# Optimization experiments

Measured on AMD Instinct MI355X. Metric: run time of the kernel, lower is better.

## Reference

```python
import jax, jax.numpy as jnp
import numpy as np

DELTA = 1e-3  # inverse-distance kernel smoothing from NEC paper
NUM_NEIGHBOURS = 50


def setup_inputs() -> dict:
    key = jax.random.key(0)
    k1, k2, k3 = jax.random.split(key, 3)
    B, C, D = 1024, 500000, 64
    return {
        "keys": jax.random.normal(k1, (B, D), dtype=jnp.float32),
        "table_keys": jax.random.normal(k2, (C, D), dtype=jnp.float32),
        "table_values": jax.random.normal(k3, (C,), dtype=jnp.float32),
    }


def reference(keys, table_keys, table_values):
    # Brute-force kNN search: squared L2 distances [B, C]
    d2 = (
        jnp.sum(keys * keys, axis=1, keepdims=True)
        - 2.0 * (keys @ table_keys.T)
        + jnp.sum(table_keys * table_keys, axis=1)[None, :]
    )
    _, idx = jax.lax.top_k(-d2, NUM_NEIGHBOURS)  # [B, K] smallest distances

    neighbours = table_keys[idx]  # [B, K, D] gather
    # recompute exact squared distances against gathered neighbours
    sq = jnp.sum((keys[:, None, :] - neighbours) ** 2, axis=2)  # [B, K]
    w = 1.0 / (sq + DELTA)
    w = w / jnp.sum(w, axis=1, keepdims=True)
    v = table_values[idx]  # [B, K]
    return jnp.sum(w * v, axis=1)  # [B]
```

## Files before the change

### kernel.cpp

```cpp
#include <hip/hip_runtime.h>
#include <math.h>


#define DELTA_SMOOTH 1e-3f
#define K_NEIGH 50
#define MAXCAP 8192
#define NBINS 256
#define MARGIN_T 1.5f
#define MARGIN_Q 26
#define RPB 1024
#define QTILE 512
#define SDEPTH 6
#define LW 768
#define CVL 2048
#define S_SAMP 8192
#define T_SAMP 8
#define FSAMPLE 2048
#define FTARGET 6
#define FMARGIN 0.75f
#define FQB 4

typedef __attribute__((ext_vector_type(8))) short short8;
typedef __attribute__((ext_vector_type(4))) float f32x4;
typedef __attribute__((address_space(1))) const unsigned int g_u32;
typedef __attribute__((address_space(3))) unsigned int l_u32;

__device__ __forceinline__ unsigned f2bf(float f) {
  unsigned u = __float_as_uint(f);
  return ((u + 0x7fffu + ((u >> 16) & 1u)) >> 16) & 0xffffu;
}

__global__ __launch_bounds__(512, 4) void convert_qthresh(
    const float* __restrict__ tk, uint4* __restrict__ tkbf,
    float* __restrict__ tnh2, const float* __restrict__ keys,
    unsigned short* __restrict__ dsamp, int C, int padded, int convB) {
  __shared__ __align__(16) unsigned char bstage[64 * 128];
  __shared__ float tnh_lds[64];
  int tid = threadIdx.x;

  if (blockIdx.x < (unsigned)convB) {
    int t = blockIdx.x * 512 + tid;
    int r = t >> 3;
    if (r >= padded) return;
    int c = t & 7;
    int rs = r < C ? r : C - 1;
    const float4* src = (const float4*)(tk + (size_t)rs * 64 + c * 8);
    float4 a = src[0], b = src[1];
    float sq = a.x * a.x + a.y * a.y + a.z * a.z + a.w * a.w
             + b.x * b.x + b.y * b.y + b.z * b.z + b.w * b.w;
    sq += __shfl_xor(sq, 1); sq += __shfl_xor(sq, 2); sq += __shfl_xor(sq, 4);
    if (c == 0) tnh2[r] = (r < C) ? sq * 0.5f : 3e38f;
    uint4 u;
    u.x = f2bf(a.x) | (f2bf(a.y) << 16);
    u.y = f2bf(a.z) | (f2bf(a.w) << 16);
    u.z = f2bf(b.x) | (f2bf(b.y) << 16);
    u.w = f2bf(b.z) | (f2bf(b.w) << 16);
    tkbf[(size_t)(r >> 6) * 512 + (r & 63) * 8 + (c ^ (r & 7))] = u;
    return;
  }

  int bid = blockIdx.x - convB;
  int qt = bid & 1;
  int chunk = bid >> 1;
  int qbase = qt * 512;
  int rstart = chunk * 64;
  int lane = tid & 63, wq = tid >> 6, l15 = lane & 15, quad = lane >> 4;

  int srow = tid >> 3, scol = tid & 7;
  const float* rowp = tk + (size_t)(rstart + srow) * 64 + scol * 8;
  float4 pa = *(const float4*)(rowp);
  float4 pb = *(const float4*)(rowp + 4);
  float part = pa.x * pa.x + pa.y * pa.y + pa.z * pa.z + pa.w * pa.w
             + pb.x * pb.x + pb.y * pb.y + pb.z * pb.z + pb.w * pb.w;
  part += __shfl_xor(part, 1); part += __shfl_xor(part, 2); part += __shfl_xor(part, 4);
  if (scol == 0) tnh_lds[srow] = part * 0.5f;
  uint4 u;
  u.x = f2bf(pa.x) | (f2bf(pa.y) << 16);
  u.y = f2bf(pa.z) | (f2bf(pa.w) << 16);
  u.z = f2bf(pb.x) | (f2bf(pb.y) << 16);
  u.w = f2bf(pb.z) | (f2bf(pb.w) << 16);
  *(uint4*)(bstage + (unsigned)(srow * 128 + ((scol ^ (srow & 7)) << 4))) = u;

  short8 afrag[4][2];
  #pragma unroll
  for (int mt = 0; mt < 4; ++mt) {
    const float* kp = keys + (size_t)(qbase + wq * 64 + mt * 16 + l15) * 64 + quad * 8;
    #pragma unroll
    for (int s = 0; s < 2; ++s) {
      float4 x = *(const float4*)(kp + s * 32);
      float4 y = *(const float4*)(kp + s * 32 + 4);
      short8 a;
      a[0] = (short)f2bf(x.x); a[1] = (short)f2bf(x.y);
      a[2] = (short)f2bf(x.z); a[3] = (short)f2bf(x.w);
      a[4] = (short)f2bf(y.x); a[5] = (short)f2bf(y.y);
      a[6] = (short)f2bf(y.z); a[7] = (short)f2bf(y.w);
      afrag[mt][s] = a;
    }
  }
  __syncthreads();
  f32x4 zero4 = {0.f, 0.f, 0.f, 0.f};
  #pragma unroll
  for (int half = 0; half < 2; ++half) {
    short8 b[2][2];
    #pragma unroll
    for (int tt = 0; tt < 2; ++tt) {
      int nloc = half * 32 + tt * 16 + l15;
      #pragma unroll
      for (int s = 0; s < 2; ++s) {
        int c = s * 4 + quad;
        unsigned addr = (unsigned)(nloc * 128 + ((c ^ (nloc & 7)) << 4));
        b[tt][s] = *(const short8*)(bstage + addr);
      }
    }
    f32x4 acc[4][2];
    #pragma unroll
    for (int mt = 0; mt < 4; ++mt)
      #pragma unroll
      for (int tt = 0; tt < 2; ++tt) {
        f32x4 a0 = __builtin_amdgcn_mfma_f32_16x16x32_bf16(afrag[mt][0], b[tt][0], zero4, 0, 0, 0);
        acc[mt][tt] = __builtin_amdgcn_mfma_f32_16x16x32_bf16(afrag[mt][1], b[tt][1], a0, 0, 0, 0);
      }
    #pragma unroll
    for (int tt = 0; tt < 2; ++tt) {
      int rloc = half * 32 + tt * 16 + l15;
      float tnh = tnh_lds[rloc];
      int n = rstart + rloc;
      #pragma unroll
      for (int mt = 0; mt < 4; ++mt) {
        #pragma unroll
        for (int r = 0; r < 4; ++r) {
          int ql = wq * 64 + mt * 16 + quad * 4 + r;
          int uq = (int)fmaf(tnh - acc[mt][tt][r], 512.f, 32768.f);
          uq = uq < 0 ? 0 : (uq > 65535 ? 65535 : uq);
          dsamp[(size_t)(qbase + ql) * S_SAMP + n] = (unsigned short)uq;
        }
      }
    }
  }
}

__global__ __launch_bounds__(256) void qthresh_scan(
    const unsigned short* __restrict__ dsamp, float* __restrict__ thrh,
    int* __restrict__ cnt) {
  int q = blockIdx.x;
  __shared__ unsigned hist[512];
  int tid = threadIdx.x;
  hist[tid] = 0u; hist[tid + 256] = 0u;
  __syncthreads();
  const unsigned short* dp = dsamp + (size_t)q * S_SAMP;
  for (int i = tid; i < S_SAMP; i += 256) atomicAdd(&hist[dp[i] >> 7], 1u);
  __syncthreads();
  if (tid == 0) {
    unsigned cum = 0; int bstar = 511;
    for (int b = 0; b < 512; ++b) {
      cum += hist[b];
      if (cum >= (unsigned)T_SAMP) { bstar = b; break; }
    }
    float thr = (float)(bstar + 1) * 0.5f - 128.f + MARGIN_T;
    thrh[q] = 0.5f * thr;
    cnt[q] = 0;
  }
}

__global__ __launch_bounds__(512, 4) void filter_mfma_fast(
    const uint4* __restrict__ tkbf, const float* __restrict__ keys,
    const float* __restrict__ tnh2, const float* __restrict__ thrh,
    int* __restrict__ cnt, unsigned* __restrict__ candi, int C, int cap) {
  __shared__ __align__(16) uint4 bstage[6][512];
  __shared__ float tnh_lds[RPB];
  __shared__ float thr_lds[QTILE];
  __shared__ unsigned scnt[QTILE];
  __shared__ unsigned sbuf[QTILE * SDEPTH];

  int tid = threadIdx.x;
  int qt = blockIdx.x & 1;
  int chunk = blockIdx.x >> 1;
  int qbase = qt * QTILE;
  int rstart = chunk * RPB;

  tnh_lds[tid] = tnh2[rstart + tid];
  tnh_lds[tid + 512] = tnh2[rstart + tid + 512];
  thr_lds[tid] = thrh[qbase + tid];
  scnt[tid] = 0u;

  int lane = tid & 63, wq = tid >> 6, l15 = lane & 15, quad = lane >> 4;

  short8 afrag[4][2];
  #pragma unroll
  for (int mt = 0; mt < 4; ++mt) {
    const float* kp = keys + (size_t)(qbase + wq * 64 + mt * 16 + l15) * 64 + quad * 8;
    #pragma unroll
    for (int s = 0; s < 2; ++s) {
      float4 x = *(const float4*)(kp + s * 32);
      float4 y = *(const float4*)(kp + s * 32 + 4);
      short8 a;
      a[0] = (short)f2bf(x.x); a[1] = (short)f2bf(x.y);
      a[2] = (short)f2bf(x.z); a[3] = (short)f2bf(x.w);
      a[4] = (short)f2bf(y.x); a[5] = (short)f2bf(y.y);
      a[6] = (short)f2bf(y.z); a[7] = (short)f2bf(y.w);
      afrag[mt][s] = a;
    }
  }

  __syncthreads();

  float negthr[4][4];
  #pragma unroll
  for (int mt = 0; mt < 4; ++mt)
    #pragma unroll
    for (int r = 0; r < 4; ++r)
      negthr[mt][r] = -thr_lds[wq * 64 + mt * 16 + quad * 4 + r];

  const uint4* gbase = tkbf + (size_t)(rstart >> 6) * 512;
  const int PAIRS = RPB / 128;
  #pragma unroll
  for (int s = 0; s < 2; ++s)
    __builtin_amdgcn_global_load_lds((g_u32*)(gbase + (size_t)s * 512 + tid),
                                     (l_u32*)((uint4*)&bstage[s][0] + wq * 64), 16, 0, 0);
  #pragma unroll
  for (int s = 0; s < 2; ++s)
    __builtin_amdgcn_global_load_lds((g_u32*)(gbase + (size_t)(2 + s) * 512 + tid),
                                     (l_u32*)((uint4*)&bstage[2 + s][0] + wq * 64), 16, 0, 0);

  for (int p = 0; p < PAIRS; ++p) {
    if (p < PAIRS - 1) {
      asm volatile("s_waitcnt vmcnt(2)\n\ts_barrier" ::: "memory");
    } else {
      asm volatile("s_waitcnt vmcnt(0)\n\ts_barrier" ::: "memory");
    }
    __builtin_amdgcn_sched_barrier(0);
    if (p + 2 < PAIRS) {
      #pragma unroll
      for (int s = 0; s < 2; ++s) {
        int slot = ((p + 2) % 3) * 2 + s;
        __builtin_amdgcn_global_load_lds(
            (g_u32*)(gbase + ((size_t)(p + 2) * 2 + s) * 512 + tid),
            (l_u32*)((uint4*)&bstage[slot][0] + wq * 64), 16, 0, 0);
      }
    }
    #pragma unroll
    for (int sl = 0; sl < 2; ++sl) {
      const unsigned char* buf = (const unsigned char*)&bstage[(p % 3) * 2 + sl][0];
      int itrow = p * 128 + sl * 64;
      #pragma unroll
      for (int half = 0; half < 2; ++half) {
        float tnh0 = tnh_lds[itrow + half * 32 + l15];
        float tnh1 = tnh_lds[itrow + half * 32 + 16 + l15];
        f32x4 c0 = {-tnh0, -tnh0, -tnh0, -tnh0};
        f32x4 c1 = {-tnh1, -tnh1, -tnh1, -tnh1};
        short8 b[2][2];
        #pragma unroll
        for (int tt = 0; tt < 2; ++tt) {
          int nloc = half * 32 + tt * 16 + l15;
          #pragma unroll
          for (int s = 0; s < 2; ++s) {
            int c = s * 4 + quad;
            unsigned addr = (unsigned)(nloc * 128 + ((c ^ (nloc & 7)) << 4));
            b[tt][s] = *(const short8*)(buf + addr);
          }
        }
        f32x4 acc[4][2];
        #pragma unroll
        for (int mt = 0; mt < 4; ++mt)
          #pragma unroll
          for (int tt = 0; tt < 2; ++tt) {
            f32x4 a0 = __builtin_amdgcn_mfma_f32_16x16x32_bf16(
                afrag[mt][0], b[tt][0], tt ? c1 : c0, 0, 0, 0);
            acc[mt][tt] = __builtin_amdgcn_mfma_f32_16x16x32_bf16(
                afrag[mt][1], b[tt][1], a0, 0, 0, 0);
          }
        #pragma unroll
        for (int tt = 0; tt < 2; ++tt) {
          int n = rstart + itrow + half * 32 + tt * 16 + l15;
          #pragma unroll
          for (int mt = 0; mt < 4; ++mt) {
            #pragma unroll
            for (int r = 0; r < 4; ++r) {
              float a = acc[mt][tt][r];
              if (__builtin_expect(a > negthr[mt][r], 0)) {
                int ql = wq * 64 + mt * 16 + quad * 4 + r;
                int d2q = (int)fmaf(-a, 32.f, 2048.f);
                d2q = d2q < 0 ? 0 : (d2q > 8191 ? 8191 : d2q);
                unsigned v = ((unsigned)d2q << 19) | (unsigned)n;
                unsigned pp = atomicAdd(&scnt[ql], 1u);
                if (pp < SDEPTH) {
                  sbuf[ql * SDEPTH + pp] = v;
                } else {
                  int g = atomicAdd(&cnt[qbase + ql], 1);
                  if (g < cap) candi[(size_t)(qbase + ql) * cap + g] = v;
                }
              }
            }
          }
        }
      }
    }
  }
  __syncthreads();
  int m = (int)scnt[tid];
  if (m > SDEPTH) m = SDEPTH;
  if (m > 0) {
    int base = atomicAdd(&cnt[qbase + tid], m);
    for (int j = 0; j < m; ++j) {
      int g = base + j;
      if (g < cap) candi[(size_t)(qbase + tid) * cap + g] = sbuf[tid * SDEPTH + j];
    }
  }
}

__global__ __launch_bounds__(256) void qthresh_fb(
    const float* __restrict__ keys, const float* __restrict__ tk,
    float* __restrict__ thr, float* __restrict__ qnorm, int C) {
  int q0 = blockIdx.x * FQB;
  __shared__ __align__(16) float kq[FQB * 64];
  __shared__ unsigned hist[FQB][NBINS];
  __shared__ float qn4[FQB];
  int tid = threadIdx.x;
  for (int i = tid; i < FQB * 64; i += 256) kq[i] = keys[(size_t)q0 * 64 + i];
  for (int i = tid; i < FQB * NBINS; i += 256) (&hist[0][0])[i] = 0u;
  __syncthreads();
  if (tid < FQB) {
    float s = 0.f;
    for (int j = 0; j < 64; ++j) { float v = kq[tid * 64 + j]; s += v * v; }
    qn4[tid] = s;
  }
  __syncthreads();
  int kc = tid & 3;
  const float4* kq4 = (const float4*)kq;
  float4 kf[FQB][4];
  #pragma unroll
  for (int jq = 0; jq < FQB; ++jq)
    #pragma unroll
    for (int u = 0; u < 4; ++u) kf[jq][u] = kq4[jq * 16 + kc * 4 + u];
  int S = FSAMPLE < C ? FSAMPLE : C;
  for (int r = tid >> 2; r < S; r += 64) {
    const float4* trow = (const float4*)(tk + (size_t)r * 64 + kc * 16);
    float4 t0 = trow[0], t1 = trow[1], t2 = trow[2], t3 = trow[3];
    float tn = t0.x * t0.x + t0.y * t0.y + t0.z * t0.z + t0.w * t0.w
             + t1.x * t1.x + t1.y * t1.y + t1.z * t1.z + t1.w * t1.w
             + t2.x * t2.x + t2.y * t2.y + t2.z * t2.z + t2.w * t2.w
             + t3.x * t3.x + t3.y * t3.y + t3.z * t3.z + t3.w * t3.w;
    tn += __shfl_xor(tn, 1); tn += __shfl_xor(tn, 2);
    float dot[FQB];
    #pragma unroll
    for (int jq = 0; jq < FQB; ++jq) {
      float s = kf[jq][0].x * t0.x + kf[jq][0].y * t0.y + kf[jq][0].z * t0.z + kf[jq][0].w * t0.w
              + kf[jq][1].x * t1.x + kf[jq][1].y * t1.y + kf[jq][1].z * t1.z + kf[jq][1].w * t1.w
              + kf[jq][2].x * t2.x + kf[jq][2].y * t2.y + kf[jq][2].z * t2.z + kf[jq][2].w * t2.w
              + kf[jq][3].x * t3.x + kf[jq][3].y * t3.y + kf[jq][3].z * t3.z + kf[jq][3].w * t3.w;
      s += __shfl_xor(s, 1); s += __shfl_xor(s, 2);
      dot[jq] = s;
    }
    if (kc == 0) {
      #pragma unroll
      for (int jq = 0; jq < FQB; ++jq) {
        float d2 = qn4[jq] + tn - 2.f * dot[jq];
        int b = (int)d2;
        b = b < 0 ? 0 : (b > NBINS - 1 ? NBINS - 1 : b);
        atomicAdd(&hist[jq][b], 1u);
      }
    }
  }
  __syncthreads();
  if (tid < FQB) {
    unsigned cum = 0; int bstar = NBINS - 1;
    for (int b = 0; b < NBINS; ++b) {
      cum += hist[tid][b];
      if (cum >= (unsigned)FTARGET) { bstar = b; break; }
    }
    thr[q0 + tid] = (float)(bstar + 1) + FMARGIN - qn4[tid];
    qnorm[q0 + tid] = qn4[tid];
  }
}

__global__ __launch_bounds__(512, 4) void filter_fb(
    const float* __restrict__ keys, const float* __restrict__ tk,
    const float* __restrict__ thr, const float* __restrict__ qnorm,
    int* __restrict__ cnt, unsigned* __restrict__ candi, int C, int cap) {
  __shared__ float tnstage[64];
  __shared__ float thr_lds[QTILE];
  __shared__ float qn_lds[QTILE];
  __shared__ unsigned scnt[QTILE];
  __shared__ unsigned sbuf[QTILE * SDEPTH];
  __shared__ __align__(16) unsigned char bstage[64 * 128];
  int tid = threadIdx.x;
  int qt = blockIdx.x & 1;
  int chunk = blockIdx.x >> 1;
  int qbase = qt * QTILE;
  int rstart = chunk * RPB;
  thr_lds[tid] = thr[qbase + tid];
  qn_lds[tid] = qnorm[qbase + tid];
  scnt[tid] = 0u;
  int lane = tid & 63, wq = tid >> 6, l15 = lane & 15, quad = lane >> 4;
  short8 afrag[4][2];
  #pragma unroll
  for (int mt = 0; mt < 4; ++mt) {
    const float* kp = keys + (size_t)(qbase + wq * 64 + mt * 16 + l15) * 64 + quad * 8;
    #pragma unroll
    for (int s = 0; s < 2; ++s) {
      float4 x = *(const float4*)(kp + s * 32);
      float4 y = *(const float4*)(kp + s * 32 + 4);
      short8 a;
      a[0] = (short)f2bf(x.x); a[1] = (short)f2bf(x.y);
      a[2] = (short)f2bf(x.z); a[3] = (short)f2bf(x.w);
      a[4] = (short)f2bf(y.x); a[5] = (short)f2bf(y.y);
      a[6] = (short)f2bf(y.z); a[7] = (short)f2bf(y.w);
      afrag[mt][s] = a;
    }
  }
  __syncthreads();
  float hq[4];
  #pragma unroll
  for (int mt = 0; mt < 4; ++mt) {
    float h0 = thr_lds[wq * 64 + mt * 16 + quad * 4 + 0];
    float h1 = thr_lds[wq * 64 + mt * 16 + quad * 4 + 1];
    float h2 = thr_lds[wq * 64 + mt * 16 + quad * 4 + 2];
    float h3 = thr_lds[wq * 64 + mt * 16 + quad * 4 + 3];
    hq[mt] = fmaxf(fmaxf(h0, h1), fmaxf(h2, h3));
  }
  int srow = tid >> 3, scol = tid & 7;
  unsigned sbyte = (unsigned)(srow * 128 + ((scol ^ (srow & 7)) << 4));
  const int ITERS = RPB / 64;
  int r0 = rstart + srow; if (r0 > C - 1) r0 = C - 1;
  float4 pa = *(const float4*)(tk + (size_t)r0 * 64 + scol * 8);
  float4 pb = *(const float4*)(tk + (size_t)r0 * 64 + scol * 8 + 4);
  f32x4 zero4 = {0.f, 0.f, 0.f, 0.f};
  for (int it = 0; it < ITERS; ++it) {
    float part = pa.x * pa.x + pa.y * pa.y + pa.z * pa.z + pa.w * pa.w
               + pb.x * pb.x + pb.y * pb.y + pb.z * pb.z + pb.w * pb.w;
    part += __shfl_xor(part, 1); part += __shfl_xor(part, 2); part += __shfl_xor(part, 4);
    if ((tid & 7) == 0) tnstage[srow] = part;
    uint4 u;
    u.x = f2bf(pa.x) | (f2bf(pa.y) << 16);
    u.y = f2bf(pa.z) | (f2bf(pa.w) << 16);
    u.z = f2bf(pb.x) | (f2bf(pb.y) << 16);
    u.w = f2bf(pb.z) | (f2bf(pb.w) << 16);
    *(uint4*)(bstage + sbyte) = u;
    __syncthreads();
    if (it + 1 < ITERS) {
      int rn = rstart + (it + 1) * 64 + srow; if (rn > C - 1) rn = C - 1;
      pa = *(const float4*)(tk + (size_t)rn * 64 + scol * 8);
      pb = *(const float4*)(tk + (size_t)rn * 64 + scol * 8 + 4);
    }
    #pragma unroll
    for (int half = 0; half < 2; ++half) {
      short8 b[2][2];
      #pragma unroll
      for (int tt = 0; tt < 2; ++tt) {
        int nloc = half * 32 + tt * 16 + l15;
        #pragma unroll
        for (int s = 0; s < 2; ++s) {
          int c = s * 4 + quad;
          unsigned addr = (unsigned)(nloc * 128 + ((c ^ (nloc & 7)) << 4));
          b[tt][s] = *(const short8*)(bstage + addr);
        }
      }
      f32x4 acc[4][2];
      #pragma unroll
      for (int mt = 0; mt < 4; ++mt)
        #pragma unroll
        for (int tt = 0; tt < 2; ++tt) {
          f32x4 a0 = __builtin_amdgcn_mfma_f32_16x16x32_bf16(afrag[mt][0], b[tt][0], zero4, 0, 0, 0);
          acc[mt][tt] = __builtin_amdgcn_mfma_f32_16x16x32_bf16(afrag[mt][1], b[tt][1], a0, 0, 0, 0);
        }
      #pragma unroll
      for (int tt = 0; tt < 2; ++tt) {
        float tn = tnstage[half * 32 + tt * 16 + l15];
        int n = rstart + it * 64 + half * 32 + tt * 16 + l15;
        #pragma unroll
        for (int mt = 0; mt < 4; ++mt) {
          float d0 = fmaf(-2.f, acc[mt][tt][0], tn);
          float d1 = fmaf(-2.f, acc[mt][tt][1], tn);
          float d2 = fmaf(-2.f, acc[mt][tt][2], tn);
          float d3 = fmaf(-2.f, acc[mt][tt][3], tn);
          float mn4 = fminf(fminf(d0, d1), fminf(d2, d3));
          if (mn4 < hq[mt]) {
            float dd[4] = {d0, d1, d2, d3};
            #pragma unroll
            for (int r = 0; r < 4; ++r) {
              int ql = wq * 64 + mt * 16 + quad * 4 + r;
              if (dd[r] < thr_lds[ql] && n < C) {
                float d2f = dd[r] + qn_lds[ql];
                int d2q = (int)(d2f * 16.f);
                d2q = d2q < 0 ? 0 : (d2q > 8191 ? 8191 : d2q);
                unsigned v = ((unsigned)d2q << 19) | (unsigned)n;
                unsigned p = atomicAdd(&scnt[ql], 1u);
                if (p < SDEPTH) sbuf[ql * SDEPTH + p] = v;
                else {
                  int g = atomicAdd(&cnt[qbase + ql], 1);
                  if (g < cap) candi[(size_t)(qbase + ql) * cap + g] = v;
                }
              }
            }
          }
        }
      }
    }
    __syncthreads();
  }
  int m = (int)scnt[tid];
  if (m > SDEPTH) m = SDEPTH;
  if (m > 0) {
    int base = atomicAdd(&cnt[qbase + tid], m);
    for (int j = 0; j < m; ++j) {
      int g = base + j;
      if (g < cap) candi[(size_t)(qbase + tid) * cap + g] = sbuf[tid * SDEPTH + j];
    }
  }
}

__global__ __launch_bounds__(256) void select_kernel(
    const float* __restrict__ keys, const float* __restrict__ tk,
    const float* __restrict__ tv, const int* __restrict__ cnt,
    const unsigned* __restrict__ candi, float* __restrict__ out, int cap) {
  int q = blockIdx.x;
  __shared__ unsigned cvl[CVL];
  __shared__ unsigned hist[NBINS];
  __shared__ unsigned wsum[4];
  __shared__ unsigned minq_sh;
  __shared__ int b50_sh;
  __shared__ int lidx[LW];
  __shared__ unsigned ed2[LW];
  __shared__ int m_sh;
  __shared__ float redw[4], redwv[4];
  int tid = threadIdx.x;
  int lane = tid & 63;
  int wid = tid >> 6;
  int n = cnt[q];
  if (n > cap) n = cap;
  hist[tid] = 0u;
  if (tid == 0) { minq_sh = 0xffffffffu; b50_sh = NBINS - 1; m_sh = 0; }
  __syncthreads();
  const unsigned* cv = candi + (size_t)q * cap;
  unsigned mn = 0xffffffffu;
  for (int i = tid; i < n; i += 256) {
    unsigned v = cv[i];
    if (i < CVL) cvl[i] = v;
    unsigned d = v >> 19; if (d < mn) mn = d;
  }
  #pragma unroll
  for (int off = 1; off < 64; off <<= 1) { unsigned o = __shfl_xor(mn, off); if (o < mn) mn = o; }
  if (lane == 0) atomicMin(&minq_sh, mn);
  __syncthreads();
  unsigned base = minq_sh;
  for (int i = tid; i < n; i += 256) {
    unsigned v = (i < CVL) ? cvl[i] : cv[i];
    unsigned d = (v >> 19) - base;
    unsigned b = d >> 1; if (b > NBINS - 1) b = NBINS - 1;
    atomicAdd(&hist[b], 1u);
  }
  __syncthreads();
  unsigned h = hist[tid];
  unsigned p = h;
  #pragma unroll
  for (int off = 1; off < 64; off <<= 1) {
    unsigned v = __shfl_up(p, off);
    if (lane >= off) p += v;
  }
  if (lane == 63) wsum[wid] = p;
  __syncthreads();
  unsigned add = 0;
  for (int w2 = 0; w2 < wid; ++w2) add += wsum[w2];
  p += add;
  if (p >= (unsigned)K_NEIGH && p - h < (unsigned)K_NEIGH) b50_sh = tid;
  __syncthreads();
  unsigned Tq = base + (((unsigned)(b50_sh + 1)) << 1) + MARGIN_Q;
  for (int i = tid; i < n; i += 256) {
    unsigned v = (i < CVL) ? cvl[i] : cv[i];
    if ((v >> 19) <= Tq) {
      int p2 = atomicAdd(&m_sh, 1);
      if (p2 < LW) lidx[p2] = (int)(v & 0x7ffffu);
    }
  }
  __syncthreads();
  int m = m_sh; if (m > LW) m = LW;
  float kqv = keys[(size_t)q * 64 + lane];
  for (int i0 = wid * 4; i0 < m; i0 += 16) {
    int mm = m - i0; if (mm > 4) mm = 4;
    int idx[4]; float t[4];
    for (int u = 0; u < mm; ++u) idx[u] = lidx[i0 + u];
    for (int u = 0; u < mm; ++u) t[u] = tk[(size_t)idx[u] * 64 + lane];
    for (int u = 0; u < mm; ++u) {
      float d = t[u] - kqv;
      float s = d * d;
      #pragma unroll
      for (int off = 1; off < 64; off <<= 1) s += __shfl_xor(s, off);
      if (lane == 0) ed2[i0 + u] = __float_as_uint(s);
    }
  }
  __syncthreads();
  float accw = 0.f, accwv = 0.f;
  for (int i = tid; i < m; i += 256) {
    unsigned long long key = ((unsigned long long)ed2[i] << 19) | (unsigned)lidx[i];
    int rank = 0;
    for (int j = 0; j < m; ++j) {
      unsigned long long kj = ((unsigned long long)ed2[j] << 19) | (unsigned)lidx[j];
      rank += (kj < key) ? 1 : 0;
    }
    if (rank < K_NEIGH) {
      float d2 = __uint_as_float(ed2[i]);
      float w = 1.f / (d2 + DELTA_SMOOTH);
      accw += w;
      accwv += w * tv[lidx[i]];
    }
  }
  #pragma unroll
  for (int off = 1; off < 64; off <<= 1) {
    accw += __shfl_xor(accw, off);
    accwv += __shfl_xor(accwv, off);
  }
  if (lane == 0) { redw[wid] = accw; redwv[wid] = accwv; }
  __syncthreads();
  if (tid == 0) {
    float sw = redw[0] + redw[1] + redw[2] + redw[3];
    float swv = redwv[0] + redwv[1] + redwv[2] + redwv[3];
    out[q] = swv / sw;
  }
}

extern "C" void kernel_launch(void* const* d_in, const int* in_sizes, int n_in,
                              void* d_out, int out_size, void* d_ws, size_t ws_size,
                              hipStream_t stream) {
  const float* keys = (const float*)d_in[0];
  const float* tk   = (const float*)d_in[1];
  const float* tv   = (const float*)d_in[2];
  float* out = (float*)d_out;
  int B = in_sizes[0] / 64;
  int C = in_sizes[2];

  int nchunks = (C + RPB - 1) / RPB;
  int padded = nchunks * RPB;

  char* w = (char*)d_ws;
  float* thrh = (float*)w;  w += (size_t)B * 4;
  float* qnfb = (float*)w;  w += (size_t)B * 4;
  int*   cnt  = (int*)w;    w += (size_t)B * 4;
  size_t fixed = (size_t)(w - (char*)d_ws);

  size_t tk_bytes = (size_t)padded * 128 + (size_t)padded * 4;
  size_t dsamp_bytes = (size_t)S_SAMP * (size_t)B * 2;
  size_t region = ws_size > fixed + tk_bytes ? ws_size - fixed - tk_bytes : 0;
  bool fast = region >= dsamp_bytes && region >= 2048ull * (size_t)B * 4;

  if (fast) {
    uint4* tkbf = (uint4*)w;              w += (size_t)padded * 128;
    float* tnh2 = (float*)w;              w += (size_t)padded * 4;
    unsigned short* dsamp = (unsigned short*)w;
    unsigned* candi = (unsigned*)w;
    int cap = (int)(region / (4ull * (size_t)B));
    if (cap > MAXCAP) cap = MAXCAP;
    int convB = (padded * 8 + 511) / 512;
    int qthB = (S_SAMP / 64) * 2;
    convert_qthresh<<<convB + qthB, 512, 0, stream>>>(tk, tkbf, tnh2, keys,
                                                      dsamp, C, padded, convB);
    qthresh_scan<<<B, 256, 0, stream>>>(dsamp, thrh, cnt);
    filter_mfma_fast<<<nchunks * 2, 512, 0, stream>>>(tkbf, keys, tnh2, thrh,
                                                      cnt, candi, C, cap);
    select_kernel<<<B, 256, 0, stream>>>(keys, tk, tv, cnt, candi, out, cap);
  } else {
    unsigned* candi = (unsigned*)w;
    int cap = (int)((ws_size - fixed) / (4ull * (size_t)B));
    if (cap > MAXCAP) cap = MAXCAP;
    if (cap < 1) cap = 1;
    hipMemsetAsync(cnt, 0, (size_t)B * 4, stream);
    qthresh_fb<<<B / FQB, 256, 0, stream>>>(keys, tk, thrh, qnfb, C);
    filter_fb<<<nchunks * 2, 512, 0, stream>>>(keys, tk, thrh, qnfb,
                                               cnt, candi, C, cap);
    select_kernel<<<B, 256, 0, stream>>>(keys, tk, tv, cnt, candi, out, cap);
  }
}
```

Baseline: 371.7 us.

## Fuse threshold histogram scan into sampling kernel via grid-wide spin barrier

```diff
diff --git a/kernel.cpp b/kernel.cpp
--- a/kernel.cpp
+++ b/kernel.cpp
@@ -33,13 +33,16 @@
 __global__ __launch_bounds__(512, 4) void convert_qthresh(
     const float* __restrict__ tk, uint4* __restrict__ tkbf,
     float* __restrict__ tnh2, const float* __restrict__ keys,
-    unsigned short* __restrict__ dsamp, int C, int padded, int convB) {
+    unsigned short* __restrict__ dsamp, float* __restrict__ thrh,
+    int* __restrict__ cnt, unsigned* __restrict__ syncc,
+    int C, int padded, int qthB) {
   __shared__ __align__(16) unsigned char bstage[64 * 128];
   __shared__ float tnh_lds[64];
+  __shared__ unsigned hist[512];
   int tid = threadIdx.x;
 
-  if (blockIdx.x < (unsigned)convB) {
-    int t = blockIdx.x * 512 + tid;
+  if (blockIdx.x >= (unsigned)qthB) {
+    int t = (blockIdx.x - qthB) * 512 + tid;
     int r = t >> 3;
     if (r >= padded) return;
     int c = t & 7;
@@ -59,7 +62,7 @@
     return;
   }
 
-  int bid = blockIdx.x - convB;
+  int bid = blockIdx.x;
   int qt = bid & 1;
   int chunk = bid >> 1;
   int qbase = qt * 512;
@@ -137,28 +140,34 @@
       }
     }
   }
-}
-
-__global__ __launch_bounds__(256) void qthresh_scan(
-    const unsigned short* __restrict__ dsamp, float* __restrict__ thrh,
-    int* __restrict__ cnt) {
-  int q = blockIdx.x;
-  __shared__ unsigned hist[512];
-  int tid = threadIdx.x;
-  hist[tid] = 0u; hist[tid + 256] = 0u;
-  __syncthreads();
-  const unsigned short* dp = dsamp + (size_t)q * S_SAMP;
-  for (int i = tid; i < S_SAMP; i += 256) atomicAdd(&hist[dp[i] >> 7], 1u);
+
+  __threadfence();
   __syncthreads();
   if (tid == 0) {
-    unsigned cum = 0; int bstar = 511;
-    for (int b = 0; b < 512; ++b) {
-      cum += hist[b];
-      if (cum >= (unsigned)T_SAMP) { bstar = b; break; }
-    }
-    float thr = (float)(bstar + 1) * 0.5f - 128.f + MARGIN_T;
-    thrh[q] = 0.5f * thr;
-    cnt[q] = 0;
+    atomicAdd(syncc, 1u);
+    while (atomicAdd(syncc, 0u) < (unsigned)qthB) __builtin_amdgcn_s_sleep(8);
+  }
+  __syncthreads();
+  __threadfence();
+
+  for (int g = 0; g < 4; ++g) {
+    int q = bid * 4 + g;
+    hist[tid] = 0u;
+    __syncthreads();
+    const unsigned short* dp = dsamp + (size_t)q * S_SAMP;
+    for (int i = tid; i < S_SAMP; i += 512) atomicAdd(&hist[dp[i] >> 7], 1u);
+    __syncthreads();
+    if (tid == 0) {
+      unsigned cum = 0; int bstar = 511;
+      for (int b = 0; b < 512; ++b) {
+        cum += hist[b];
+        if (cum >= (unsigned)T_SAMP) { bstar = b; break; }
+      }
+      float thr = (float)(bstar + 1) * 0.5f - 128.f + MARGIN_T;
+      thrh[q] = 0.5f * thr;
+      cnt[q] = 0;
+    }
+    __syncthreads();
   }
 }
 
@@ -635,6 +644,7 @@
   float* thrh = (float*)w;  w += (size_t)B * 4;
   float* qnfb = (float*)w;  w += (size_t)B * 4;
   int*   cnt  = (int*)w;    w += (size_t)B * 4;
+  unsigned* syncc = (unsigned*)w; w += 16;
   size_t fixed = (size_t)(w - (char*)d_ws);
 
   size_t tk_bytes = (size_t)padded * 128 + (size_t)padded * 4;
@@ -651,9 +661,9 @@
     if (cap > MAXCAP) cap = MAXCAP;
     int convB = (padded * 8 + 511) / 512;
     int qthB = (S_SAMP / 64) * 2;
-    convert_qthresh<<<convB + qthB, 512, 0, stream>>>(tk, tkbf, tnh2, keys,
-                                                      dsamp, C, padded, convB);
-    qthresh_scan<<<B, 256, 0, stream>>>(dsamp, thrh, cnt);
+    hipMemsetAsync(syncc, 0, 4, stream);
+    convert_qthresh<<<qthB + convB, 512, 0, stream>>>(
+        tk, tkbf, tnh2, keys, dsamp, thrh, cnt, syncc, C, padded, qthB);
     filter_mfma_fast<<<nchunks * 2, 512, 0, stream>>>(tkbf, keys, tnh2, thrh,
                                                       cnt, candi, C, cap);
     select_kernel<<<B, 256, 0, stream>>>(keys, tk, tv, cnt, candi, out, cap);
```

Measured after the change: 530.8 us. 1.43x slower.
